# Optimization experiments

Measured on AMD Instinct MI355X. Metric: run time of the kernel, lower is better.

Reference implementation:

```python
import jax, jax.numpy as jnp
import numpy as np

EPS = 1e-5
NUM_HEADS = 8
KEY_CH = 512
VAL_CH = 512


def instance_norm(x):
    # x: [B, N, C]; torch InstanceNorm1d normalizes over the length dim (N) per (b, c), no affine
    m = jnp.mean(x, axis=1, keepdims=True)
    v = jnp.var(x, axis=1, keepdims=True)
    return (x - m) / jnp.sqrt(v + EPS)


def setup_inputs() -> dict:
    key = jax.random.key(0)
    ks = jax.random.split(key, 16)
    B, HW, D, NL, LC = 8, 16384, 512, 20, 768
    s = 0.02
    inp = {
        "x": jax.random.normal(ks[0], (B, HW, D), dtype=jnp.float32),
        "l": jax.random.normal(ks[1], (B, NL, LC), dtype=jnp.float32),
        "l_mask": jnp.ones((B, NL), dtype=jnp.float32),
        # vis_project conv1d(dim->dim)
        "Wv": jax.random.normal(ks[2], (D, D), dtype=jnp.float32) * s,
        "bv": jnp.zeros((D,), dtype=jnp.float32),
        # f_query conv1d(v_in->key)
        "Wq": jax.random.normal(ks[3], (D, KEY_CH), dtype=jnp.float32) * s,
        "bq": jnp.zeros((KEY_CH,), dtype=jnp.float32),
        # f_key conv1d(l_in->key)
        "Wk": jax.random.normal(ks[4], (LC, KEY_CH), dtype=jnp.float32) * s,
        "bk": jnp.zeros((KEY_CH,), dtype=jnp.float32),
        # f_value conv1d(l_in->value)
        "Wval": jax.random.normal(ks[5], (LC, VAL_CH), dtype=jnp.float32) * s,
        "bval": jnp.zeros((VAL_CH,), dtype=jnp.float32),
        # W conv1d(value->out)
        "Ww": jax.random.normal(ks[6], (VAL_CH, VAL_CH), dtype=jnp.float32) * s,
        "bw": jnp.zeros((VAL_CH,), dtype=jnp.float32),
        # project_mm conv1d(value->value)
        "Wm": jax.random.normal(ks[7], (VAL_CH, VAL_CH), dtype=jnp.float32) * s,
        "bm": jnp.zeros((VAL_CH,), dtype=jnp.float32),
    }
    return inp


def reference(x, l, l_mask, Wv, bv, Wq, bq, Wk, bk, Wval, bval, Ww, bw, Wm, bm):
    B, HW, _ = x.shape
    n_l = l.shape[1]
    H = NUM_HEADS
    dk = KEY_CH // H
    dv = VAL_CH // H

    # vis_project: 1x1 conv + GELU (exact) + dropout(p=0)
    vis = jax.nn.gelu(x @ Wv + bv, approximate=False)  # [B, HW, D]

    # SpatialImageLanguageAttention
    q = instance_norm(x @ Wq + bq)          # [B, HW, Kc], InstanceNorm over HW
    k = l @ Wk + bk                          # [B, n_l, Kc]
    v = l @ Wval + bval                      # [B, n_l, Vc]

    q = q.reshape(B, HW, H, dk)              # bqhd
    k = k.reshape(B, n_l, H, dk)             # bkhd
    v = v.reshape(B, n_l, H, dv)             # bkhd

    sim = jnp.einsum("bqhd,bkhd->bhqk", q, k) * (KEY_CH ** -0.5)
    sim = jax.nn.softmax(sim, axis=-1)       # softmax over short language seq
    out = jnp.einsum("bhqk,bkhd->bqhd", sim, v).reshape(B, HW, VAL_CH)

    lang = instance_norm(out @ Ww + bw)      # [B, HW, Vc]

    # gated fusion + project_mm
    mm = vis * lang
    mm = jax.nn.gelu(mm @ Wm + bm, approximate=False)
    return mm
```

## Files before the change

### kernel.cpp

```cpp
#include <hip/hip_runtime.h>

#define HWN 16384
#define DMODEL 512
#define NLANG 20
#define LCH 768
#define NB 8
#define MTOT (NB*HWN)
#define NHEADS 8

typedef float floatx4 __attribute__((ext_vector_type(4)));
typedef short short8 __attribute__((ext_vector_type(8)));

__device__ __forceinline__ float bflo(unsigned u){ return __uint_as_float(u << 16); }
__device__ __forceinline__ float bfhi(unsigned u){ return __uint_as_float(u & 0xffff0000u); }
__device__ __forceinline__ unsigned short f2bf(float f){
  unsigned u = __float_as_uint(f);
  u += 0x7fffu + ((u >> 16) & 1u);
  return (unsigned short)(u >> 16);
}
__device__ __forceinline__ unsigned pack2(float a, float b){
  return (unsigned)f2bf(a) | ((unsigned)f2bf(b) << 16);
}
__device__ __forceinline__ float geluf(float v){
  float t = v * v;
  float u2 = v * fmaf(t, -0.0713548162f, -1.5957691216f);
  float e = __expf(u2);
  return v * __builtin_amdgcn_rcpf(1.0f + e);
}
__device__ __forceinline__ void stage16(const void* g, void* l){
  __builtin_amdgcn_global_load_lds(
      (const __attribute__((address_space(1))) void*)g,
      (__attribute__((address_space(3))) void*)l, 16, 0, 0);
}
__device__ __forceinline__ int tslot(int c){ return ((c & 7) << 3) | (c >> 3); }

__global__ void prep_w(const float* __restrict__ Wv, const float* __restrict__ Wq,
                       const float* __restrict__ Ww, const float* __restrict__ Wm,
                       unsigned short* __restrict__ wcatT, unsigned short* __restrict__ wwT,
                       unsigned short* __restrict__ wmT)
{
  int i = blockIdx.x * 256 + threadIdx.x;
  if (i < 1024 * 512) {
    int n = i >> 9, k = i & 511;
    float v = (n < 512) ? Wv[k * 512 + n] : Wq[k * 512 + (n - 512)];
    wcatT[i] = f2bf(v);
  } else {
    int j = i - 1024 * 512;
    if (j < 512 * 512) { int n = j >> 9, k = j & 511; wwT[j] = f2bf(Ww[k * 512 + n]); }
    else { j -= 512 * 512; int n = j >> 9, k = j & 511; wmT[j] = f2bf(Wm[k * 512 + n]); }
  }
}

__global__ void xcvt(const float* __restrict__ x, unsigned short* __restrict__ xb)
{
  size_t i = ((size_t)blockIdx.x * 256 + threadIdx.x) * 8;
  float4 a = *reinterpret_cast<const float4*>(&x[i]);
  float4 b = *reinterpret_cast<const float4*>(&x[i + 4]);
  uint4 d;
  d.x = pack2(a.x, a.y); d.y = pack2(a.z, a.w);
  d.z = pack2(b.x, b.y); d.w = pack2(b.z, b.w);
  *reinterpret_cast<uint4*>(&xb[i]) = d;
}

__global__ void mmk(const unsigned short* __restrict__ y, const unsigned short* __restrict__ vis,
                    const float* __restrict__ lma, const float* __restrict__ lmb,
                    unsigned short* __restrict__ mm)
{
  size_t i = ((size_t)blockIdx.x * 256 + threadIdx.x) * 8;
  int c = (int)(i & 511);
  int b = (int)(i >> 23);
  uint4 yv = *reinterpret_cast<const uint4*>(&y[i]);
  uint4 vv = *reinterpret_cast<const uint4*>(&vis[i]);
  const float* Ap = &lma[b * 512 + c];
  const float* Bp = &lmb[b * 512 + c];
  float4 a0 = *reinterpret_cast<const float4*>(Ap);
  float4 a1 = *reinterpret_cast<const float4*>(Ap + 4);
  float4 b0 = *reinterpret_cast<const float4*>(Bp);
  float4 b1 = *reinterpret_cast<const float4*>(Bp + 4);
  float m0 = bflo(vv.x) * (bflo(yv.x) * a0.x + b0.x);
  float m1 = bfhi(vv.x) * (bfhi(yv.x) * a0.y + b0.y);
  float m2 = bflo(vv.y) * (bflo(yv.y) * a0.z + b0.z);
  float m3 = bfhi(vv.y) * (bfhi(yv.y) * a0.w + b0.w);
  float m4 = bflo(vv.z) * (bflo(yv.z) * a1.x + b1.x);
  float m5 = bfhi(vv.z) * (bfhi(yv.z) * a1.y + b1.y);
  float m6 = bflo(vv.w) * (bflo(yv.w) * a1.z + b1.z);
  float m7 = bfhi(vv.w) * (bfhi(yv.w) * a1.w + b1.w);
  uint4 d;
  d.x = pack2(m0, m1); d.y = pack2(m2, m3);
  d.z = pack2(m4, m5); d.w = pack2(m6, m7);
  *reinterpret_cast<uint4*>(&mm[i]) = d;
}

__global__ void prep_kv(const float* __restrict__ l, const float* __restrict__ Wk,
                        const float* __restrict__ bk, const float* __restrict__ Wval,
                        const float* __restrict__ bval,
                        float* __restrict__ kraw, unsigned short* __restrict__ vb)
{
  int i = blockIdx.x * 256 + threadIdx.x;
  int which = i / (NB * NLANG * 512);
  int j = i - which * (NB * NLANG * 512);
  int bt = j >> 9;
  int c = j & 511;
  const float* W = which ? Wval : Wk;
  float acc = which ? bval[c] : bk[c];
  const float* lr = l + (size_t)bt * LCH;
  for (int p = 0; p < LCH; p++) acc = fmaf(lr[p], W[p * 512 + c], acc);
  if (which) {
    int cnk = c >> 3, e = c & 7;
    vb[bt * 512 + tslot(cnk) * 8 + e] = f2bf(acc);
  } else {
    kraw[j] = acc;
  }
}

__global__ void kprep(const float* __restrict__ qsum, const float* __restrict__ qsq,
                      const float* __restrict__ kraw, unsigned short* __restrict__ kp,
                      float* __restrict__ offG)
{
  int blk = blockIdx.x; int b = blk / NLANG, t = blk - b * NLANG;
  int lane = threadIdx.x;
  float offp = 0.f;
  float vals[8];
  #pragma unroll
  for (int e = 0; e < 8; e++) {
    int c = lane * 8 + e;
    float mean = qsum[b * 512 + c] * (1.f / 16384.f);
    float var  = qsq[b * 512 + c] * (1.f / 16384.f) - mean * mean;
    float inv  = rsqrtf(var + 1e-5f);
    float a = inv * 0.044194173824159216f;
    float kv = kraw[((size_t)(b * NLANG + t)) * 512 + c];
    vals[e] = kv * a;
    offp += (-mean * a) * kv;
  }
  unsigned u0 = pack2(vals[0], vals[1]);
  unsigned u1 = pack2(vals[2], vals[3]);
  unsigned u2 = pack2(vals[4], vals[5]);
  unsigned u3 = pack2(vals[6], vals[7]);
  uint4 uu = make_uint4(u0, u1, u2, u3);
  *reinterpret_cast<uint4*>(&kp[((size_t)(b * NLANG + t)) * 512 + tslot(lane) * 8]) = uu;
  offp += __shfl_xor(offp, 1);
  offp += __shfl_xor(offp, 2);
  offp += __shfl_xor(offp, 4);
  if ((lane & 7) == 0) offG[(b * 8 + (lane >> 3)) * NLANG + t] = offp;
}

__global__ void lmk(const float* __restrict__ ysum, const float* __restrict__ ysq,
                    float* __restrict__ lma, float* __restrict__ lmb)
{
  int i = blockIdx.x * 256 + threadIdx.x;
  if (i < NB * 512) {
    float mean = ysum[i] * (1.f / 16384.f);
    float var  = ysq[i] * (1.f / 16384.f) - mean * mean;
    float inv  = rsqrtf(var + 1e-5f);
    lma[i] = inv; lmb[i] = -mean * inv;
  }
}

__global__ __launch_bounds__(256, 2) void attn_k(
    const unsigned short* __restrict__ kp, const unsigned short* __restrict__ vbg,
    const float* __restrict__ offG, unsigned short* __restrict__ qb)
{
  __shared__ __align__(16) unsigned short kps[NLANG * 512];
  __shared__ __align__(16) unsigned short vbs[NLANG * 512];
  __shared__ __align__(16) unsigned short qs[32 * 512];
  __shared__ float offs[NHEADS * NLANG];
  int tid = threadIdx.x, bid = blockIdx.x;
  int b = bid >> 9;
  int row0 = (bid & 511) * 32;
  size_t base = (size_t)b * (NLANG * 512);
  const uint4* kg = reinterpret_cast<const uint4*>(kp + base);
  const uint4* vg = reinterpret_cast<const uint4*>(vbg + base);
  uint4* kl = reinterpret_cast<uint4*>(kps);
  uint4* vl = reinterpret_cast<uint4*>(vbs);
  #pragma unroll
  for (int i = 0; i < 5; i++) { int o = i * 256 + tid; kl[o] = kg[o]; vl[o] = vg[o]; }
  if (tid < NHEADS * NLANG) offs[tid] = offG[b * (NHEADS * NLANG) + tid];

  size_t grow0 = (size_t)b * HWN + row0;
  #pragma unroll
  for (int i = 0; i < 8; i++) {
    int g = i * 256 + tid;
    int row = g >> 6, c = g & 63;
    uint4 d = *reinterpret_cast<const uint4*>(&qb[(grow0 + row) * 512 + c * 8]);
    *reinterpret_cast<uint4*>(&qs[row * 512 + tslot(c) * 8]) = d;
  }
  __syncthreads();

  int r = tid >> 3, h = tid & 7;
  float sim[NLANG];
  #pragma unroll
  for (int t = 0; t < NLANG; t++) sim[t] = offs[h * NLANG + t];
  #pragma unroll
  for (int j = 0; j < 8; j++) {
    uint4 qv = *reinterpret_cast<const uint4*>(&qs[r * 512 + (j * 8 + h) * 8]);
    float q0 = bflo(qv.x), q1 = bfhi(qv.x), q2 = bflo(qv.y), q3 = bfhi(qv.y);
    float q4 = bflo(qv.z), q5 = bfhi(qv.z), q6 = bflo(qv.w), q7 = bfhi(qv.w);
    #pragma unroll
    for (int t = 0; t < NLANG; t++) {
      uint4 kv = *reinterpret_cast<const uint4*>(&kps[t * 512 + (j * 8 + h) * 8]);
      float a = sim[t];
      a = fmaf(q0, bflo(kv.x), a); a = fmaf(q1, bfhi(kv.x), a);
      a = fmaf(q2, bflo(kv.y), a); a = fmaf(q3, bfhi(kv.y), a);
      a = fmaf(q4, bflo(kv.z), a); a = fmaf(q5, bfhi(kv.z), a);
      a = fmaf(q6, bflo(kv.w), a); a = fmaf(q7, bfhi(kv.w), a);
      sim[t] = a;
    }
  }
  float mx = sim[0];
  #pragma unroll
  for (int t = 1; t < NLANG; t++) mx = fmaxf(mx, sim[t]);
  float s = 0.f;
  #pragma unroll
  for (int t = 0; t < NLANG; t++) { float e = __expf(sim[t] - mx); sim[t] = e; s += e; }
  float invs = 1.f / s;
  #pragma unroll
  for (int t = 0; t < NLANG; t++) sim[t] *= invs;

  float o[8][8];
  #pragma unroll
  for (int a2 = 0; a2 < 8; a2++)
    #pragma unroll
    for (int b2 = 0; b2 < 8; b2++) o[a2][b2] = 0.f;
  #pragma unroll
  for (int t = 0; t < NLANG; t++) {
    float p = sim[t];
    #pragma unroll
    for (int j = 0; j < 8; j++) {
      uint4 v4 = *reinterpret_cast<const uint4*>(&vbs[t * 512 + (j * 8 + h) * 8]);
      o[j][0] = fmaf(p, bflo(v4.x), o[j][0]); o[j][1] = fmaf(p, bfhi(v4.x), o[j][1]);
      o[j][2] = fmaf(p, bflo(v4.y), o[j][2]); o[j][3] = fmaf(p, bfhi(v4.y), o[j][3]);
      o[j][4] = fmaf(p, bflo(v4.z), o[j][4]); o[j][5] = fmaf(p, bfhi(v4.z), o[j][5]);
      o[j][6] = fmaf(p, bflo(v4.w), o[j][6]); o[j][7] = fmaf(p, bfhi(v4.w), o[j][7]);
    }
  }
  #pragma unroll
  for (int j = 0; j < 8; j++) {
    uint4 u;
    u.x = pack2(o[j][0], o[j][1]); u.y = pack2(o[j][2], o[j][3]);
    u.z = pack2(o[j][4], o[j][5]); u.w = pack2(o[j][6], o[j][7]);
    *reinterpret_cast<uint4*>(&qs[r * 512 + (j * 8 + h) * 8]) = u;
  }
  __syncthreads();
  #pragma unroll
  for (int i = 0; i < 8; i++) {
    int g = i * 256 + tid;
    int row = g >> 6, c = g & 63;
    uint4 d = *reinterpret_cast<const uint4*>(&qs[row * 512 + tslot(c) * 8]);
    *reinterpret_cast<uint4*>(&qb[(grow0 + row) * 512 + c * 8]) = d;
  }
}

template<int MODE>
__global__ __launch_bounds__(256) void gemm_k(
    const unsigned short* __restrict__ A,
    const unsigned short* __restrict__ Bw,
    const float* __restrict__ bias0, const float* __restrict__ bias1,
    unsigned short* __restrict__ Out0, unsigned short* __restrict__ Out1,
    float* __restrict__ OutF,
    float* __restrict__ sum1, float* __restrict__ sum2)
{
  constexpr int GN  = (MODE == 0) ? 8 : 4;
  constexpr int NWG = (MODE == 0) ? 8192 : 4096;
  __shared__ __align__(16) unsigned short SM[6 * 128 * 32];

  int raw = blockIdx.x;
  int lid = (raw & 7) * (NWG / 8) + (raw >> 3);
  int tileN = lid & (GN - 1);
  int tileM = lid / GN;
  int tm128 = tileM * 128;
  int b512 = (tileM >> 7) * 512;
  int tid = threadIdx.x;
  int wave = tid >> 6, lane = tid & 63;
  int wr = (wave >> 1) * 64, wc = (wave & 1) * 64;
  int r15 = lane & 15, kcg = lane >> 4;

  floatx4 acc[4][4];
  floatx4 zz = {0.f, 0.f, 0.f, 0.f};
  #pragma unroll
  for (int m = 0; m < 4; m++)
    #pragma unroll
    for (int n = 0; n < 4; n++) acc[m][n] = zz;

  const unsigned short* Arow = A + (size_t)tm128 * 512;
  const unsigned short* Brow = Bw + (size_t)(tileN * 128) * 512;

  auto stage = [&](int kt, int s) {
    int k0 = kt * 32;
    unsigned short* As = SM + s * 4096;
    unsigned short* Bs = SM + (3 + s) * 4096;
    #pragma unroll
    for (int i = 0; i < 2; i++) {
      int idx = i * 256 + tid;
      int row = idx >> 2;
      int c = (idx & 3) ^ ((row >> 1) & 3);
      stage16(&Arow[(size_t)row * 512 + k0 + c * 8],
              &As[(i * 256 + wave * 64) * 8]);
    }
    #pragma unroll
    for (int i = 0; i < 2; i++) {
      int idx = i * 256 + tid;
      int row = idx >> 2;
      int c = (idx & 3) ^ ((row >> 1) & 3);
      stage16(&Brow[(size_t)row * 512 + k0 + c * 8],
              &Bs[(i * 256 + wave * 64) * 8]);
    }
  };

  stage(0, 0);
  stage(1, 1);
  #pragma unroll
  for (int kt = 0; kt < 16; kt++) {
    int s = kt % 3;
    __builtin_amdgcn_sched_barrier(0);
    if (kt < 15) asm volatile("s_waitcnt vmcnt(4) lgkmcnt(0)\n\ts_barrier" ::: "memory");
    else         asm volatile("s_waitcnt vmcnt(0) lgkmcnt(0)\n\ts_barrier" ::: "memory");
    __builtin_amdgcn_sched_barrier(0);
    if (kt + 2 < 16) stage(kt + 2, (kt + 2) % 3);
    const unsigned short* As = SM + s * 4096;
    const unsigned short* Bs = SM + (3 + s) * 4096;
    short8 af[4], bfv[4];
    #pragma unroll
    for (int m = 0; m < 4; m++) {
      int R = wr + m * 16 + r15;
      af[m] = *reinterpret_cast<const short8*>(&As[R * 32 + (kcg ^ ((R >> 1) & 3)) * 8]);
    }
    #pragma unroll
    for (int n = 0; n < 4; n++) {
      int R = wc + n * 16 + r15;
      bfv[n] = *reinterpret_cast<const short8*>(&Bs[R * 32 + (kcg ^ ((R >> 1) & 3)) * 8]);
    }
    #pragma unroll
    for (int m = 0; m < 4; m++)
      #pragma unroll
      for (int n = 0; n < 4; n++)
        acc[m][n] = __builtin_amdgcn_mfma_f32_16x16x32_bf16(af[m], bfv[n], acc[m][n], 0, 0, 0);
  }

  __syncthreads();

  if constexpr (MODE == 2) {
    int baseM = tm128 + wr + (lane >> 4) * 4;
    #pragma unroll
    for (int n = 0; n < 4; n++) {
      int gcol = tileN * 128 + wc + n * 16 + r15;
      #pragma unroll
      for (int m = 0; m < 4; m++) {
        int rowb = baseM + m * 16;
        #pragma unroll
        for (int j = 0; j < 4; j++) {
          float v = geluf(acc[m][n][j] + bias0[gcol]);
          OutF[(size_t)(rowb + j) * 512 + gcol] = v;
        }
      }
    }
  } else {
    unsigned short* C = SM;
    int baseR = wr + (lane >> 4) * 4;
    #pragma unroll
    for (int n = 0; n < 4; n++) {
      int lcol = wc + n * 16 + r15;
      int gcol = tileN * 128 + lcol;
      float s1 = 0.f, s2 = 0.f;
      #pragma unroll
      for (int m = 0; m < 4; m++) {
        #pragma unroll
        for (int j = 0; j < 4; j++) {
          int lrow = baseR + m * 16 + j;
          float v = acc[m][n][j];
          if constexpr (MODE == 0) {
            if (tileN < 4) {
              v = geluf(v + bias0[gcol]);
            } else {
              v += bias1[gcol - 512];
              s1 += v; s2 += v * v;
            }
          } else {
            v += bias0[gcol];
            s1 += v; s2 += v * v;
          }
          C[lrow * 128 + (lcol ^ (((lrow >> 2) & 3) << 4))] = f2bf(v);
        }
      }
      bool doStats = (MODE == 1) || (tileN >= 4);
      if (doStats) {
        s1 += __shfl_xor(s1, 16); s1 += __shfl_xor(s1, 32);
        s2 += __shfl_xor(s2, 16); s2 += __shfl_xor(s2, 32);
        if (lane < 16) {
          int c = (MODE == 0) ? (gcol - 512) : gcol;
          atomicAdd(&sum1[b512 + c], s1);
          atomicAdd(&sum2[b512 + c], s2);
        }
      }
    }
    __syncthreads();
    unsigned short* Og;
    int colbase;
    if constexpr (MODE == 0) {
      if (tileN < 4) { Og = Out0; colbase = tileN * 128; }
      else           { Og = Out1; colbase = (tileN - 4) * 128; }
    } else {
      Og = Out0; colbase = tileN * 128;
    }
    #pragma unroll
    for (int t = 0; t < 8; t++) {
      int cid = t * 256 + tid;
      int row = cid >> 4, cc = cid & 15;
      uint4 d = *reinterpret_cast<const uint4*>(&C[row * 128 + ((cc * 8) ^ (((row >> 2) & 3) << 4))]);
      *reinterpret_cast<uint4*>(&Og[(size_t)(tm128 + row) * 512 + colbase + cc * 8]) = d;
    }
  }
}

extern "C" void kernel_launch(void* const* d_in, const int* in_sizes, int n_in,
                              void* d_out, int out_size, void* d_ws, size_t ws_size,
                              hipStream_t stream)
{
  const float* x   = (const float*)d_in[0];
  const float* l   = (const float*)d_in[1];
  const float* Wv  = (const float*)d_in[3];
  const float* bv  = (const float*)d_in[4];
  const float* Wq  = (const float*)d_in[5];
  const float* bq  = (const float*)d_in[6];
  const float* Wk  = (const float*)d_in[7];
  const float* bk  = (const float*)d_in[8];
  const float* Wva = (const float*)d_in[9];
  const float* bva = (const float*)d_in[10];
  const float* Ww  = (const float*)d_in[11];
  const float* bw  = (const float*)d_in[12];
  const float* Wm  = (const float*)d_in[13];
  const float* bm  = (const float*)d_in[14];

  char* w = (char*)d_ws;
  size_t o = 0;
  auto alloc = [&](size_t bytes) { size_t r = o; o += (bytes + 255) & ~(size_t)255; return r; };
  size_t WCATT = alloc(1024 * 512 * 2);
  size_t WWT   = alloc(512 * 512 * 2);
  size_t WMT   = alloc(512 * 512 * 2);
  size_t KRAW  = alloc((size_t)NB * NLANG * 512 * 4);
  size_t VB    = alloc((size_t)NB * NLANG * 512 * 2);
  size_t KP    = alloc((size_t)NB * NLANG * 512 * 2);
  size_t OFFW  = alloc((size_t)NB * NHEADS * NLANG * 4);
  size_t STATS = alloc((size_t)4 * NB * 512 * 4);
  size_t LMA   = alloc((size_t)NB * 512 * 4);
  size_t LMB   = alloc((size_t)NB * 512 * 4);
  size_t XB    = alloc((size_t)MTOT * 512 * 2);
  size_t VIS   = alloc((size_t)MTOT * 512 * 2);
  size_t QBUF  = alloc((size_t)MTOT * 512 * 2);
  size_t YBUF  = alloc((size_t)MTOT * 512 * 2);

  float* qsum = (float*)(w + STATS);
  float* qsq  = qsum + NB * 512;
  float* ysum = qsq + NB * 512;
  float* ysq  = ysum + NB * 512;

  hipMemsetAsync(w + STATS, 0, (size_t)4 * NB * 512 * 4, stream);
  prep_w<<<4096, 256, 0, stream>>>(Wv, Wq, Ww, Wm,
      (unsigned short*)(w + WCATT), (unsigned short*)(w + WWT), (unsigned short*)(w + WMT));
  xcvt<<<32768, 256, 0, stream>>>(x, (unsigned short*)(w + XB));
  prep_kv<<<640, 256, 0, stream>>>(l, Wk, bk, Wva, bva,
      (float*)(w + KRAW), (unsigned short*)(w + VB));
  gemm_k<0><<<8192, 256, 0, stream>>>((const unsigned short*)(w + XB),
      (const unsigned short*)(w + WCATT), bv, bq,
      (unsigned short*)(w + VIS), (unsigned short*)(w + QBUF), nullptr, qsum, qsq);
  kprep<<<160, 64, 0, stream>>>(qsum, qsq, (const float*)(w + KRAW),
      (unsigned short*)(w + KP), (float*)(w + OFFW));
  attn_k<<<4096, 256, 0, stream>>>((const unsigned short*)(w + KP),
      (const unsigned short*)(w + VB), (const float*)(w + OFFW),
      (unsigned short*)(w + QBUF));
  gemm_k<1><<<4096, 256, 0, stream>>>((const unsigned short*)(w + QBUF),
      (const unsigned short*)(w + WWT), bw, nullptr,
      (unsigned short*)(w + YBUF), nullptr, nullptr, ysum, ysq);
  lmk<<<16, 256, 0, stream>>>(ysum, ysq, (float*)(w + LMA), (float*)(w + LMB));
  mmk<<<32768, 256, 0, stream>>>((const unsigned short*)(w + YBUF),
      (const unsigned short*)(w + VIS), (const float*)(w + LMA), (const float*)(w + LMB),
      (unsigned short*)(w + XB));
  gemm_k<2><<<4096, 256, 0, stream>>>((const unsigned short*)(w + XB),
      (const unsigned short*)(w + WMT), bm, nullptr,
      nullptr, nullptr, (float*)d_out, nullptr, nullptr);
}
```

Measured before the change: 987.7 us.

## Replace first fused GEMM with 256x256-tile 8-wave kernel and double-buffered LDS pipeline

Adds a new gemm8 kernel for the combined x@[Wv|Wq] projection that uses 256x256 output tiles, 512 threads (8 waves) and 128 KB of double-buffered shared memory with XOR-swizzled staging. Loads for the next K-slice are issued while the MFMAs for the current slice run, with explicit barriers and s_setprio around the MFMA blocks. The GELU on the vis half and the InstanceNorm statistics on the q half stay in the epilogue. Larger tiles cut global and LDS traffic per FLOP, at the cost of more shared memory per block and higher register pressure, which limits occupancy to two blocks.

```diff
diff --git a/kernel.cpp b/kernel.cpp
--- a/kernel.cpp
+++ b/kernel.cpp
@@ -250,6 +250,151 @@
   }
 }
 
+__global__ __launch_bounds__(512, 2) void gemm8(
+    const unsigned short* __restrict__ A,
+    const unsigned short* __restrict__ Bw,
+    const float* __restrict__ bias0, const float* __restrict__ bias1,
+    unsigned short* __restrict__ Out0, unsigned short* __restrict__ Out1,
+    float* __restrict__ sum1, float* __restrict__ sum2)
+{
+  constexpr int NWG = 2048;
+  __shared__ __align__(16) unsigned short SM[65536];
+
+  int raw = blockIdx.x;
+  int lid = (raw & 7) * (NWG / 8) + (raw >> 3);
+  int tileN = lid & 3;
+  int tileM = lid >> 2;
+  int tm = tileM * 256;
+  int b512 = (tileM >> 6) * 512;
+  int tid = threadIdx.x;
+  int wave = tid >> 6, lane = tid & 63;
+  int wm = wave >> 2, wn = wave & 3;
+  int r15 = lane & 15, kcg = lane >> 4;
+
+  floatx4 acc[8][4];
+  floatx4 zz = {0.f, 0.f, 0.f, 0.f};
+  #pragma unroll
+  for (int m = 0; m < 8; m++)
+    #pragma unroll
+    for (int n = 0; n < 4; n++) acc[m][n] = zz;
+
+  const unsigned short* Ab = A + (size_t)tm * 512;
+  const unsigned short* Bb = Bw + (size_t)(tileN * 256) * 512;
+
+  auto stageH = [&](int t, int X, int h) {
+    const unsigned short* G = X ? Bb : Ab;
+    unsigned short* L = SM + X * 32768 + ((t & 1) * 2 + h) * 8192;
+    #pragma unroll
+    for (int i = 0; i < 2; i++) {
+      int c = i * 512 + tid;
+      int row = c >> 3, c8 = c & 7;
+      stage16(&G[(size_t)(h * 128 + row) * 512 + t * 64 + (c8 ^ (row & 7)) * 8],
+              &L[c * 8]);
+    }
+  };
+
+  stageH(0, 0, 0); stageH(0, 0, 1); stageH(0, 1, 0); stageH(0, 1, 1);
+  stageH(1, 0, 0); stageH(1, 0, 1); stageH(1, 1, 0); stageH(1, 1, 1);
+  __builtin_amdgcn_sched_barrier(0);
+  asm volatile("s_waitcnt vmcnt(8)\n\ts_barrier" ::: "memory");
+  __builtin_amdgcn_sched_barrier(0);
+
+  for (int t = 0; t < 8; t++) {
+    const unsigned short* Asl = SM + ((t & 1) * 2 + wm) * 8192;
+    const unsigned short* Bsl = SM + 32768 + ((t & 1) * 2 + (wn >> 1)) * 8192;
+    int brow0 = (wn & 1) * 64;
+    #pragma unroll
+    for (int p = 0; p < 4; p++) {
+      int qm = p >> 1, qn = p & 1;
+      if (t >= 1 && t < 7) {
+        if (p == 0)      { stageH(t + 1, 0, 0); stageH(t + 1, 0, 1); }
+        else if (p == 1) { stageH(t + 1, 1, 0); stageH(t + 1, 1, 1); }
+      }
+      short8 af[4][2], bf[2][2];
+      #pragma unroll
+      for (int mf = 0; mf < 4; mf++) {
+        int row = (qm * 4 + mf) * 16 + r15;
+        #pragma unroll
+        for (int kk = 0; kk < 2; kk++)
+          af[mf][kk] = *reinterpret_cast<const short8*>(
+              &Asl[row * 64 + ((kk * 4 + kcg) ^ (row & 7)) * 8]);
+      }
+      #pragma unroll
+      for (int nf = 0; nf < 2; nf++) {
+        int row = brow0 + (qn * 2 + nf) * 16 + r15;
+        #pragma unroll
+        for (int kk = 0; kk < 2; kk++)
+          bf[nf][kk] = *reinterpret_cast<const short8*>(
+              &Bsl[row * 64 + ((kk * 4 + kcg) ^ (row & 7)) * 8]);
+      }
+      __builtin_amdgcn_s_setprio(1);
+      #pragma unroll
+      for (int kk = 0; kk < 2; kk++)
+        #pragma unroll
+        for (int mf = 0; mf < 4; mf++)
+          #pragma unroll
+          for (int nf = 0; nf < 2; nf++)
+            acc[qm * 4 + mf][qn * 2 + nf] = __builtin_amdgcn_mfma_f32_16x16x32_bf16(
+                af[mf][kk], bf[nf][kk], acc[qm * 4 + mf][qn * 2 + nf], 0, 0, 0);
+      __builtin_amdgcn_s_setprio(0);
+      if (p < 3) {
+        __builtin_amdgcn_sched_barrier(0);
+        __builtin_amdgcn_s_barrier();
+        __builtin_amdgcn_sched_barrier(0);
+      }
+    }
+    __builtin_amdgcn_sched_barrier(0);
+    if (t < 7) asm volatile("s_waitcnt vmcnt(0)\n\ts_barrier" ::: "memory");
+    __builtin_amdgcn_sched_barrier(0);
+  }
+  __syncthreads();
+
+  unsigned short* C = SM;
+  int baseR = wm * 128 + kcg * 4;
+  #pragma unroll
+  for (int nf = 0; nf < 4; nf++) {
+    int lcol = wn * 64 + nf * 16 + r15;
+    int gcol = tileN * 256 + lcol;
+    float s1 = 0.f, s2 = 0.f;
+    #pragma unroll
+    for (int mf = 0; mf < 8; mf++) {
+      #pragma unroll
+      for (int j = 0; j < 4; j++) {
+        int lrow = baseR + mf * 16 + j;
+        float v = acc[mf][nf][j];
+        if (tileN < 2) {
+          v = geluf(v + bias0[gcol]);
+        } else {
+          v += bias1[gcol - 512];
+          s1 += v; s2 += v * v;
+        }
+        C[lrow * 256 + (lcol ^ (((lrow >> 2) & 3) << 4))] = f2bf(v);
+      }
+    }
+    if (tileN >= 2) {
+      s1 += __shfl_xor(s1, 16); s1 += __shfl_xor(s1, 32);
+      s2 += __shfl_xor(s2, 16); s2 += __shfl_xor(s2, 32);
+      if (lane < 16) {
+        atomicAdd(&sum1[b512 + gcol - 512], s1);
+        atomicAdd(&sum2[b512 + gcol - 512], s2);
+      }
+    }
+  }
+  __syncthreads();
+  unsigned short* Og;
+  int colbase;
+  if (tileN < 2) { Og = Out0; colbase = tileN * 256; }
+  else           { Og = Out1; colbase = (tileN - 2) * 256; }
+  #pragma unroll
+  for (int tt = 0; tt < 16; tt++) {
+    int cid = tt * 512 + tid;
+    int row = cid >> 5, cc = cid & 31;
+    uint4 d = *reinterpret_cast<const uint4*>(
+        &C[row * 256 + ((cc * 8) ^ (((row >> 2) & 3) << 4))]);
+    *reinterpret_cast<uint4*>(&Og[(size_t)(tm + row) * 512 + colbase + cc * 8]) = d;
+  }
+}
+
 template<int MODE>
 __global__ __launch_bounds__(256) void gemm_k(
     const unsigned short* __restrict__ A,
@@ -459,9 +604,9 @@
   xcvt<<<32768, 256, 0, stream>>>(x, (unsigned short*)(w + XB));
   prep_kv<<<640, 256, 0, stream>>>(l, Wk, bk, Wva, bva,
       (float*)(w + KRAW), (unsigned short*)(w + VB));
-  gemm_k<0><<<8192, 256, 0, stream>>>((const unsigned short*)(w + XB),
+  gemm8<<<2048, 512, 0, stream>>>((const unsigned short*)(w + XB),
       (const unsigned short*)(w + WCATT), bv, bq,
-      (unsigned short*)(w + VIS), (unsigned short*)(w + QBUF), nullptr, qsum, qsq);
+      (unsigned short*)(w + VIS), (unsigned short*)(w + QBUF), qsum, qsq);
   kprep<<<160, 64, 0, stream>>>(qsum, qsq, (const float*)(w + KRAW),
       (unsigned short*)(w + KP), (float*)(w + OFFW));
   attn_k<<<4096, 256, 0, stream>>>((const unsigned short*)(w + KP),
```

Measured after the change: 1.021 ms. 1.03x slower.

## Fold value projection into W per batch so attention feeds GEMM with probabilities

Applied to the files above, without the earlier changes.

Precomputes per-batch matrices W2 = V_h @ Ww_h (zero-padded to 256 over head×token), so the attention kernel writes only softmax probabilities (256 bf16 per row) and the second GEMM consumes them with K=256 instead of 512. This drops the P·V accumulation and the 512-wide output write from attn_k, and halves the K depth of the W GEMM. In exchange it adds a small w2prep kernel, batch-dependent B operand indexing, and padded zero columns. Rounding changes because probabilities and the fused V·Ww products are stored in bf16.

```diff
diff --git a/kernel.cpp b/kernel.cpp
--- a/kernel.cpp
+++ b/kernel.cpp
@@ -35,9 +35,8 @@
 __device__ __forceinline__ int tslot(int c){ return ((c & 7) << 3) | (c >> 3); }
 
 __global__ void prep_w(const float* __restrict__ Wv, const float* __restrict__ Wq,
-                       const float* __restrict__ Ww, const float* __restrict__ Wm,
-                       unsigned short* __restrict__ wcatT, unsigned short* __restrict__ wwT,
-                       unsigned short* __restrict__ wmT)
+                       const float* __restrict__ Wm,
+                       unsigned short* __restrict__ wcatT, unsigned short* __restrict__ wmT)
 {
   int i = blockIdx.x * 256 + threadIdx.x;
   if (i < 1024 * 512) {
@@ -46,8 +45,8 @@
     wcatT[i] = f2bf(v);
   } else {
     int j = i - 1024 * 512;
-    if (j < 512 * 512) { int n = j >> 9, k = j & 511; wwT[j] = f2bf(Ww[k * 512 + n]); }
-    else { j -= 512 * 512; int n = j >> 9, k = j & 511; wmT[j] = f2bf(Wm[k * 512 + n]); }
+    int n = j >> 9, k = j & 511;
+    wmT[j] = f2bf(Wm[k * 512 + n]);
   }
 }
 
@@ -105,12 +104,27 @@
   float acc = which ? bval[c] : bk[c];
   const float* lr = l + (size_t)bt * LCH;
   for (int p = 0; p < LCH; p++) acc = fmaf(lr[p], W[p * 512 + c], acc);
-  if (which) {
-    int cnk = c >> 3, e = c & 7;
-    vb[bt * 512 + tslot(cnk) * 8 + e] = f2bf(acc);
-  } else {
-    kraw[j] = acc;
-  }
+  if (which) vb[j] = f2bf(acc);
+  else       kraw[j] = acc;
+}
+
+__global__ void w2prep(const unsigned short* __restrict__ vb, const float* __restrict__ Ww,
+                       unsigned short* __restrict__ w2t)
+{
+  int i = blockIdx.x * 256 + threadIdx.x;
+  int k = i & 255;
+  int n = (i >> 8) & 511;
+  int b = i >> 17;
+  int t = k & 31, h = k >> 5;
+  float acc = 0.f;
+  if (t < NLANG) {
+    const unsigned short* vr = &vb[(size_t)(b * NLANG + t) * 512 + h * 64];
+    const float* wr = &Ww[(size_t)(h * 64) * 512 + n];
+    #pragma unroll 8
+    for (int d = 0; d < 64; d++)
+      acc = fmaf(__uint_as_float((unsigned)vr[d] << 16), wr[d * 512], acc);
+  }
+  w2t[(size_t)(b * 512 + n) * 256 + k] = f2bf(acc);
 }
 
 __global__ void kprep(const float* __restrict__ qsum, const float* __restrict__ qsq,
@@ -156,12 +170,11 @@
   }
 }
 
-__global__ __launch_bounds__(256, 2) void attn_k(
-    const unsigned short* __restrict__ kp, const unsigned short* __restrict__ vbg,
-    const float* __restrict__ offG, unsigned short* __restrict__ qb)
+__global__ __launch_bounds__(256, 3) void attn_k(
+    const unsigned short* __restrict__ kp, const float* __restrict__ offG,
+    const unsigned short* __restrict__ qb, unsigned short* __restrict__ pb)
 {
   __shared__ __align__(16) unsigned short kps[NLANG * 512];
-  __shared__ __align__(16) unsigned short vbs[NLANG * 512];
   __shared__ __align__(16) unsigned short qs[32 * 512];
   __shared__ float offs[NHEADS * NLANG];
   int tid = threadIdx.x, bid = blockIdx.x;
@@ -169,11 +182,9 @@
   int row0 = (bid & 511) * 32;
   size_t base = (size_t)b * (NLANG * 512);
   const uint4* kg = reinterpret_cast<const uint4*>(kp + base);
-  const uint4* vg = reinterpret_cast<const uint4*>(vbg + base);
   uint4* kl = reinterpret_cast<uint4*>(kps);
-  uint4* vl = reinterpret_cast<uint4*>(vbs);
-  #pragma unroll
-  for (int i = 0; i < 5; i++) { int o = i * 256 + tid; kl[o] = kg[o]; vl[o] = vg[o]; }
+  #pragma unroll
+  for (int i = 0; i < 5; i++) { int o = i * 256 + tid; kl[o] = kg[o]; }
   if (tid < NHEADS * NLANG) offs[tid] = offG[b * (NHEADS * NLANG) + tid];
 
   size_t grow0 = (size_t)b * HWN + row0;
@@ -216,41 +227,19 @@
   #pragma unroll
   for (int t = 0; t < NLANG; t++) sim[t] *= invs;
 
-  float o[8][8];
-  #pragma unroll
-  for (int a2 = 0; a2 < 8; a2++)
-    #pragma unroll
-    for (int b2 = 0; b2 < 8; b2++) o[a2][b2] = 0.f;
-  #pragma unroll
-  for (int t = 0; t < NLANG; t++) {
-    float p = sim[t];
-    #pragma unroll
-    for (int j = 0; j < 8; j++) {
-      uint4 v4 = *reinterpret_cast<const uint4*>(&vbs[t * 512 + (j * 8 + h) * 8]);
-      o[j][0] = fmaf(p, bflo(v4.x), o[j][0]); o[j][1] = fmaf(p, bfhi(v4.x), o[j][1]);
-      o[j][2] = fmaf(p, bflo(v4.y), o[j][2]); o[j][3] = fmaf(p, bfhi(v4.y), o[j][3]);
-      o[j][4] = fmaf(p, bflo(v4.z), o[j][4]); o[j][5] = fmaf(p, bfhi(v4.z), o[j][5]);
-      o[j][6] = fmaf(p, bflo(v4.w), o[j][6]); o[j][7] = fmaf(p, bfhi(v4.w), o[j][7]);
-    }
-  }
-  #pragma unroll
-  for (int j = 0; j < 8; j++) {
-    uint4 u;
-    u.x = pack2(o[j][0], o[j][1]); u.y = pack2(o[j][2], o[j][3]);
-    u.z = pack2(o[j][4], o[j][5]); u.w = pack2(o[j][6], o[j][7]);
-    *reinterpret_cast<uint4*>(&qs[r * 512 + (j * 8 + h) * 8]) = u;
-  }
-  __syncthreads();
-  #pragma unroll
-  for (int i = 0; i < 8; i++) {
-    int g = i * 256 + tid;
-    int row = g >> 6, c = g & 63;
-    uint4 d = *reinterpret_cast<const uint4*>(&qs[row * 512 + tslot(c) * 8]);
-    *reinterpret_cast<uint4*>(&qb[(grow0 + row) * 512 + c * 8]) = d;
-  }
-}
-
-template<int MODE>
+  unsigned uu[16];
+  #pragma unroll
+  for (int j = 0; j < 10; j++) uu[j] = pack2(sim[2 * j], sim[2 * j + 1]);
+  #pragma unroll
+  for (int j = 10; j < 16; j++) uu[j] = 0u;
+  size_t prow = (grow0 + r) * 256 + h * 32;
+  #pragma unroll
+  for (int j = 0; j < 4; j++)
+    *reinterpret_cast<uint4*>(&pb[prow + j * 8]) =
+        make_uint4(uu[4 * j], uu[4 * j + 1], uu[4 * j + 2], uu[4 * j + 3]);
+}
+
+template<int MODE, int KD>
 __global__ __launch_bounds__(256) void gemm_k(
     const unsigned short* __restrict__ A,
     const unsigned short* __restrict__ Bw,
@@ -261,6 +250,7 @@
 {
   constexpr int GN  = (MODE == 0) ? 8 : 4;
   constexpr int NWG = (MODE == 0) ? 8192 : 4096;
+  constexpr int KT  = KD / 32;
   __shared__ __align__(16) unsigned short SM[6 * 128 * 32];
 
   int raw = blockIdx.x;
@@ -281,8 +271,10 @@
     #pragma unroll
     for (int n = 0; n < 4; n++) acc[m][n] = zz;
 
-  const unsigned short* Arow = A + (size_t)tm128 * 512;
-  const unsigned short* Brow = Bw + (size_t)(tileN * 128) * 512;
+  const unsigned short* Arow = A + (size_t)tm128 * KD;
+  const unsigned short* Brow = Bw +
+      ((MODE == 1) ? (size_t)(tileM >> 7) * 512 * KD : (size_t)0) +
+      (size_t)(tileN * 128) * KD;
 
   auto stage = [&](int kt, int s) {
     int k0 = kt * 32;
@@ -293,7 +285,7 @@
       int idx = i * 256 + tid;
       int row = idx >> 2;
       int c = (idx & 3) ^ ((row >> 1) & 3);
-      stage16(&Arow[(size_t)row * 512 + k0 + c * 8],
+      stage16(&Arow[(size_t)row * KD + k0 + c * 8],
               &As[(i * 256 + wave * 64) * 8]);
     }
     #pragma unroll
@@ -301,7 +293,7 @@
       int idx = i * 256 + tid;
       int row = idx >> 2;
       int c = (idx & 3) ^ ((row >> 1) & 3);
-      stage16(&Brow[(size_t)row * 512 + k0 + c * 8],
+      stage16(&Brow[(size_t)row * KD + k0 + c * 8],
               &Bs[(i * 256 + wave * 64) * 8]);
     }
   };
@@ -309,13 +301,13 @@
   stage(0, 0);
   stage(1, 1);
   #pragma unroll
-  for (int kt = 0; kt < 16; kt++) {
+  for (int kt = 0; kt < KT; kt++) {
     int s = kt % 3;
     __builtin_amdgcn_sched_barrier(0);
-    if (kt < 15) asm volatile("s_waitcnt vmcnt(4) lgkmcnt(0)\n\ts_barrier" ::: "memory");
-    else         asm volatile("s_waitcnt vmcnt(0) lgkmcnt(0)\n\ts_barrier" ::: "memory");
+    if (kt < KT - 1) asm volatile("s_waitcnt vmcnt(4) lgkmcnt(0)\n\ts_barrier" ::: "memory");
+    else             asm volatile("s_waitcnt vmcnt(0) lgkmcnt(0)\n\ts_barrier" ::: "memory");
     __builtin_amdgcn_sched_barrier(0);
-    if (kt + 2 < 16) stage(kt + 2, (kt + 2) % 3);
+    if (kt + 2 < KT) stage(kt + 2, (kt + 2) % 3);
     const unsigned short* As = SM + s * 4096;
     const unsigned short* Bs = SM + (3 + s) * 4096;
     short8 af[4], bfv[4];
@@ -434,8 +426,8 @@
   size_t o = 0;
   auto alloc = [&](size_t bytes) { size_t r = o; o += (bytes + 255) & ~(size_t)255; return r; };
   size_t WCATT = alloc(1024 * 512 * 2);
-  size_t WWT   = alloc(512 * 512 * 2);
   size_t WMT   = alloc(512 * 512 * 2);
+  size_t W2T   = alloc((size_t)NB * 512 * 256 * 2);
   size_t KRAW  = alloc((size_t)NB * NLANG * 512 * 4);
   size_t VB    = alloc((size_t)NB * NLANG * 512 * 2);
   size_t KP    = alloc((size_t)NB * NLANG * 512 * 2);
@@ -446,6 +438,7 @@
   size_t XB    = alloc((size_t)MTOT * 512 * 2);
   size_t VIS   = alloc((size_t)MTOT * 512 * 2);
   size_t QBUF  = alloc((size_t)MTOT * 512 * 2);
+  size_t PB    = alloc((size_t)MTOT * 256 * 2);
   size_t YBUF  = alloc((size_t)MTOT * 512 * 2);
 
   float* qsum = (float*)(w + STATS);
@@ -454,27 +447,29 @@
   float* ysq  = ysum + NB * 512;
 
   hipMemsetAsync(w + STATS, 0, (size_t)4 * NB * 512 * 4, stream);
-  prep_w<<<4096, 256, 0, stream>>>(Wv, Wq, Ww, Wm,
-      (unsigned short*)(w + WCATT), (unsigned short*)(w + WWT), (unsigned short*)(w + WMT));
+  prep_w<<<3072, 256, 0, stream>>>(Wv, Wq, Wm,
+      (unsigned short*)(w + WCATT), (unsigned short*)(w + WMT));
   xcvt<<<32768, 256, 0, stream>>>(x, (unsigned short*)(w + XB));
   prep_kv<<<640, 256, 0, stream>>>(l, Wk, bk, Wva, bva,
       (float*)(w + KRAW), (unsigned short*)(w + VB));
-  gemm_k<0><<<8192, 256, 0, stream>>>((const unsigned short*)(w + XB),
+  w2prep<<<4096, 256, 0, stream>>>((const unsigned short*)(w + VB), Ww,
+      (unsigned short*)(w + W2T));
+  gemm_k<0, 512><<<8192, 256, 0, stream>>>((const unsigned short*)(w + XB),
       (const unsigned short*)(w + WCATT), bv, bq,
       (unsigned short*)(w + VIS), (unsigned short*)(w + QBUF), nullptr, qsum, qsq);
   kprep<<<160, 64, 0, stream>>>(qsum, qsq, (const float*)(w + KRAW),
       (unsigned short*)(w + KP), (float*)(w + OFFW));
   attn_k<<<4096, 256, 0, stream>>>((const unsigned short*)(w + KP),
-      (const unsigned short*)(w + VB), (const float*)(w + OFFW),
-      (unsigned short*)(w + QBUF));
-  gemm_k<1><<<4096, 256, 0, stream>>>((const unsigned short*)(w + QBUF),
-      (const unsigned short*)(w + WWT), bw, nullptr,
+      (const float*)(w + OFFW), (const unsigned short*)(w + QBUF),
+      (unsigned short*)(w + PB));
+  gemm_k<1, 256><<<4096, 256, 0, stream>>>((const unsigned short*)(w + PB),
+      (const unsigned short*)(w + W2T), bw, nullptr,
       (unsigned short*)(w + YBUF), nullptr, nullptr, ysum, ysq);
   lmk<<<16, 256, 0, stream>>>(ysum, ysq, (float*)(w + LMA), (float*)(w + LMB));
   mmk<<<32768, 256, 0, stream>>>((const unsigned short*)(w + YBUF),
       (const unsigned short*)(w + VIS), (const float*)(w + LMA), (const float*)(w + LMB),
       (unsigned short*)(w + XB));
-  gemm_k<2><<<4096, 256, 0, stream>>>((const unsigned short*)(w + XB),
+  gemm_k<2, 512><<<4096, 256, 0, stream>>>((const unsigned short*)(w + XB),
       (const unsigned short*)(w + WMT), bm, nullptr,
       nullptr, nullptr, (float*)d_out, nullptr, nullptr);
 }
```

New measurement: 861.0 us. -12.8%, faster.
